# Kernel tuning notes

Hardware: AMD Instinct MI355X
Metric: run time of the kernel (lower is better)

## Reference

```python
import jax, jax.numpy as jnp
import numpy as np

HIDDEN = 768
TMPL = 128  # template tokens stripped from x/xi
LN_EPS = 1e-5


def _layernorm(h, gamma, beta):
    mu = jnp.mean(h, axis=-1, keepdims=True)
    var = jnp.mean((h - mu) ** 2, axis=-1, keepdims=True)
    return (h - mu) * jax.lax.rsqrt(var + LN_EPS) * gamma + beta


def setup_inputs() -> dict:
    key = jax.random.key(0)
    ks = jax.random.split(key, 7)
    B, NT, LX, C = 32, 320, 704, HIDDEN
    s = C ** -0.5  # scale params so activations stay O(1)
    return {
        "T": jax.random.normal(ks[0], (B, NT, C), jnp.float32),
        "x": jax.random.normal(ks[1], (B, LX, C), jnp.float32),
        "xi": jax.random.normal(ks[2], (B, LX, C), jnp.float32),
        "Wq": jax.random.normal(ks[3], (C, C), jnp.float32) * s,
        "Wk": jax.random.normal(ks[4], (C, C), jnp.float32) * s,
        "Wv": jax.random.normal(ks[5], (C, C), jnp.float32) * s,
        "Wout": jax.random.normal(ks[6], (C, C), jnp.float32) * s,
        "gamma": jnp.ones((C,), jnp.float32),
        "beta": jnp.zeros((C,), jnp.float32),
    }


def reference(T, x, xi, Wq, Wk, Wv, Wout, gamma, beta):
    scale = T.shape[-1] ** -0.5
    xs = x[:, TMPL:]    # [B, N, C]
    xis = xi[:, TMPL:]  # [B, N, C]

    q = jnp.einsum("btc,cd->btd", T, Wq)
    k = jnp.einsum("bnc,cd->bnd", xs, Wk)
    ki = jnp.einsum("bnc,cd->bnd", xis, Wk)
    v = jnp.einsum("bnc,cd->bnd", xs, Wv)
    vi = jnp.einsum("bnc,cd->bnd", xis, Wv)

    aw = jax.nn.softmax(jnp.einsum("btd,bnd->btn", q, k) * scale, axis=-1)   # [B,Nt,N]
    awi = jax.nn.softmax(jnp.einsum("btd,bnd->btn", q, ki) * scale, axis=-1)  # [B,Nt,N]

    D = aw - awi
    num_rows = jnp.float32(D.shape[1])
    ones_cnt = jnp.sum(D > 0, axis=1).astype(jnp.float32)   # [B,N]
    half_cnt = jnp.sum(D == 0, axis=1).astype(jnp.float32)  # [B,N]
    rgb_ratio = (ones_cnt / num_rows)[..., None]   # [B,N,1]
    eq_ratio = (half_cnt / num_rows)[..., None]    # [B,N,1]
    tir_ratio = 1.0 - rgb_ratio - eq_ratio

    x_s = v * (rgb_ratio + eq_ratio) + vi * (tir_ratio + eq_ratio)  # [B,N,C]

    x_out = jnp.einsum("btn,bnc->btc", aw, v) @ Wout
    xi_out = jnp.einsum("btn,bnc->btc", awi, vi) @ Wout
    T_new = _layernorm(T + x_out + xi_out, gamma, beta)
    return x_s, T_new
```

## Files before the change

kernel.cpp:

```cpp
#include <hip/hip_runtime.h>

#define BB   32
#define NT   320
#define LX   704
#define TMPL 128
#define NS   576
#define CC   768
#define NS2  1152
#define LN_EPS 1e-5f

typedef __attribute__((ext_vector_type(8))) short short8;
typedef __attribute__((ext_vector_type(4))) float f32x4;
typedef unsigned long long u64;

typedef __attribute__((address_space(3))) void as3_void;
typedef __attribute__((address_space(1))) void as1_void;
#define GLDS16(g, l) __builtin_amdgcn_global_load_lds((const as1_void*)(g), (as3_void*)(l), 16, 0, 0)

__device__ __forceinline__ unsigned short f2bf(float f) {
    union { float f; unsigned u; } v; v.f = f;
    unsigned r = v.u + 0x7FFFu + ((v.u >> 16) & 1u);
    return (unsigned short)(r >> 16);
}
__device__ __forceinline__ float bf2f(unsigned short h) {
    union { unsigned u; float f; } v; v.u = ((unsigned)h) << 16;
    return v.f;
}

__device__ __forceinline__ float block_sum256(float v) {
    __shared__ float sm[4];
    #pragma unroll
    for (int o = 32; o > 0; o >>= 1) v += __shfl_down(v, o, 64);
    __syncthreads();
    if ((threadIdx.x & 63) == 0) sm[threadIdx.x >> 6] = v;
    __syncthreads();
    return sm[0] + sm[1] + sm[2] + sm[3];
}
__device__ __forceinline__ float block_max256(float v) {
    __shared__ float sm[4];
    #pragma unroll
    for (int o = 32; o > 0; o >>= 1) v = fmaxf(v, __shfl_down(v, o, 64));
    __syncthreads();
    if ((threadIdx.x & 63) == 0) sm[threadIdx.x >> 6] = v;
    __syncthreads();
    return fmaxf(fmaxf(sm[0], sm[1]), fmaxf(sm[2], sm[3]));
}

template<bool F32OUT>
__device__ __forceinline__ void gemm64_core(const short* __restrict__ Ab,
                                            const short* __restrict__ Bb,
                                            void* __restrict__ Cb,
                                            int N, int K, float alpha)
{
    __shared__ short As[64 * 32];
    __shared__ short Bs[128 * 32];
    const int m0 = blockIdx.y * 64;
    const int n0 = blockIdx.x * 128;
    const int tid  = threadIdx.x;
    const int lane = tid & 63;
    const int w    = tid >> 6;
    const int wr   = (w >> 1) * 32;
    const int wc   = (w & 1) * 64;

    const int srow = tid >> 2;
    const int g    = ((tid & 3) ^ ((srow >> 1) & 3)) * 8;
    const short* gA  = Ab + (long)(m0 + srow) * K + g;
    const short* gB0 = Bb + (long)(n0 + srow) * K + g;
    const short* gB1 = gB0 + (long)64 * K;
    short* lA  = As + tid * 8;
    short* lB0 = Bs + tid * 8;
    short* lB1 = Bs + 2048 + tid * 8;

    const int fl = lane & 15;
    const int ch = lane >> 4;

    f32x4 acc[2][4] = {};

    for (int k0 = 0; k0 < K; k0 += 32) {
        GLDS16(gA  + k0, lA);
        GLDS16(gB0 + k0, lB0);
        GLDS16(gB1 + k0, lB1);
        __syncthreads();

        short8 af[2], bfv[4];
        #pragma unroll
        for (int mt = 0; mt < 2; ++mt) {
            int row = wr + mt * 16 + fl;
            af[mt] = *(const short8*)(As + row * 32 + ((ch ^ ((row >> 1) & 3)) * 8));
        }
        #pragma unroll
        for (int nt = 0; nt < 4; ++nt) {
            int row = wc + nt * 16 + fl;
            bfv[nt] = *(const short8*)(Bs + row * 32 + ((ch ^ ((row >> 1) & 3)) * 8));
        }
        #pragma unroll
        for (int mt = 0; mt < 2; ++mt)
            #pragma unroll
            for (int nt = 0; nt < 4; ++nt)
                acc[mt][nt] = __builtin_amdgcn_mfma_f32_16x16x32_bf16(
                    af[mt], bfv[nt], acc[mt][nt], 0, 0, 0);
        __syncthreads();
    }

    float* Cf = (float*)Cb;
    unsigned short* Ch = (unsigned short*)Cb;
    const int rq = (lane >> 4) * 4;
    #pragma unroll
    for (int mt = 0; mt < 2; ++mt) {
        #pragma unroll
        for (int r = 0; r < 4; ++r) {
            long ro = (long)(m0 + wr + mt * 16 + rq + r) * N + n0 + wc + fl;
            #pragma unroll
            for (int nt = 0; nt < 4; ++nt) {
                float val = acc[mt][nt][r] * alpha;
                if (F32OUT) Cf[ro + nt * 16] = val;
                else        Ch[ro + nt * 16] = f2bf(val);
            }
        }
    }
}

template<bool F32OUT>
__global__ __launch_bounds__(256) void gemm64(
    const short* __restrict__ A, const short* __restrict__ Bt, void* __restrict__ C,
    int N, int K, long sA, long sB, long sC, float alpha)
{
    const int b = blockIdx.z;
    void* Cb = F32OUT ? (void*)((float*)C + (long)b * sC)
                      : (void*)((unsigned short*)C + (long)b * sC);
    gemm64_core<F32OUT>(A + (long)b * sA, Bt + (long)b * sB, Cb, N, K, alpha);
}

__global__ __launch_bounds__(256) void proj4(
    const short* __restrict__ xsb, const short* __restrict__ xisb,
    const short* __restrict__ WkT, const short* __restrict__ WvT,
    unsigned short* __restrict__ kkb, unsigned short* __restrict__ vvb)
{
    const int which = blockIdx.z & 3;
    const int b     = blockIdx.z >> 2;
    const short* A  = ((which & 1) ? xisb : xsb) + (long)b * NS * CC;
    const short* Bt = (which & 2) ? WvT : WkT;
    unsigned short* C = ((which & 2) ? vvb : kkb)
                        + (long)b * NS2 * CC + (long)(which & 1) * NS * CC;
    gemm64_core<false>(A, Bt, C, CC, CC, 1.f);
}

__global__ void conv_in(const float* __restrict__ T, const float* __restrict__ x,
                        const float* __restrict__ xi,
                        unsigned short* __restrict__ Tb, unsigned short* __restrict__ xsb,
                        unsigned short* __restrict__ xisb)
{
    const int which = blockIdx.y;
    long i4 = ((long)blockIdx.x * 256 + threadIdx.x) * 4;
    const float* src; unsigned short* dst; long total; int rows, off, rpb;
    if (which == 0) { src = T;  dst = Tb;   total = (long)BB * NT * CC; rows = NT; off = 0;    rpb = NT; }
    else if (which == 1) { src = x;  dst = xsb;  total = (long)BB * NS * CC; rows = LX; off = TMPL; rpb = NS; }
    else            { src = xi; dst = xisb; total = (long)BB * NS * CC; rows = LX; off = TMPL; rpb = NS; }
    if (i4 >= total) return;
    int c   = (int)(i4 % CC);
    long rw = i4 / CC;
    int t   = (int)(rw % rpb);
    int b   = (int)(rw / rpb);
    const float4 f = *(const float4*)(src + ((long)b * rows + off + t) * CC + c);
    ushort4 o;
    o.x = f2bf(f.x); o.y = f2bf(f.y); o.z = f2bf(f.z); o.w = f2bf(f.w);
    *(ushort4*)(dst + i4) = o;
}

__global__ void conv_wt4(const float* __restrict__ Wq, const float* __restrict__ Wk,
                         const float* __restrict__ Wv, const float* __restrict__ Wo,
                         unsigned short* __restrict__ WqT, unsigned short* __restrict__ WkT,
                         unsigned short* __restrict__ WvT, unsigned short* __restrict__ WoT)
{
    const float* W; unsigned short* WT;
    switch (blockIdx.z) {
        case 0: W = Wq; WT = WqT; break;
        case 1: W = Wk; WT = WkT; break;
        case 2: W = Wv; WT = WvT; break;
        default: W = Wo; WT = WoT; break;
    }
    __shared__ float tile[32][33];
    const int c0 = blockIdx.x * 32, r0 = blockIdx.y * 32;
    const int tx = threadIdx.x & 31, ty = threadIdx.x >> 5;
    #pragma unroll
    for (int i = 0; i < 4; ++i)
        tile[ty + 8 * i][tx] = W[(long)(r0 + ty + 8 * i) * CC + c0 + tx];
    __syncthreads();
    #pragma unroll
    for (int i = 0; i < 4; ++i)
        WT[(long)(c0 + ty + 8 * i) * CC + r0 + tx] = f2bf(tile[tx][ty + 8 * i]);
}

__global__ void trans_vv(const unsigned short* __restrict__ vvb, unsigned short* __restrict__ vvT)
{
    __shared__ unsigned short tile[32][34];
    const int b = blockIdx.z;
    const int n0 = blockIdx.x * 32, c0 = blockIdx.y * 32;
    const int tx = threadIdx.x & 31, ty = threadIdx.x >> 5;
    const long ib = (long)b * NS2 * CC;
    #pragma unroll
    for (int i = 0; i < 4; ++i)
        tile[ty + 8 * i][tx] = vvb[ib + (long)(n0 + ty + 8 * i) * CC + c0 + tx];
    __syncthreads();
    #pragma unroll
    for (int i = 0; i < 4; ++i)
        vvT[ib + (long)(c0 + ty + 8 * i) * NS2 + n0 + tx] = tile[tx][ty + 8 * i];
}

__global__ void softmax_pack(const float* __restrict__ P, unsigned short* __restrict__ Pb,
                             u64* __restrict__ posm, u64* __restrict__ eqm)
{
    const long r = blockIdx.x;
    const float* p = P + r * NS2;
    const int tid = threadIdx.x;

    float a0 = p[tid], a1 = p[tid + 256], a2 = (tid < 64) ? p[tid + 512] : -1e30f;
    float m1 = block_max256(fmaxf(fmaxf(a0, a1), a2));
    float e0 = __expf(a0 - m1), e1 = __expf(a1 - m1), e2 = (tid < 64) ? __expf(a2 - m1) : 0.f;
    float s1 = block_sum256(e0 + e1 + e2);
    float i1 = 1.f / s1;
    e0 *= i1; e1 *= i1; e2 *= i1;

    const float* q = p + NS;
    float b0 = q[tid], b1 = q[tid + 256], b2 = (tid < 64) ? q[tid + 512] : -1e30f;
    float m2 = block_max256(fmaxf(fmaxf(b0, b1), b2));
    float f0 = __expf(b0 - m2), f1 = __expf(b1 - m2), f2v = (tid < 64) ? __expf(b2 - m2) : 0.f;
    float s2 = block_sum256(f0 + f1 + f2v);
    float i2 = 1.f / s2;
    f0 *= i2; f1 *= i2; f2v *= i2;

    unsigned short* ob = Pb + r * NS2;
    ob[tid] = f2bf(e0); ob[tid + 256] = f2bf(e1);
    if (tid < 64) ob[tid + 512] = f2bf(e2);
    ob[NS + tid] = f2bf(f0); ob[NS + tid + 256] = f2bf(f1);
    if (tid < 64) ob[NS + tid + 512] = f2bf(f2v);

    u64* pm = posm + r * 9;
    u64* em = eqm  + r * 9;
    const int wv = tid >> 6;
    float d0 = e0 - f0, d1 = e1 - f1, d2 = e2 - f2v;
    u64 P0 = __ballot(d0 > 0.f), E0 = __ballot(d0 == 0.f);
    if ((tid & 63) == 0) { pm[wv] = P0; em[wv] = E0; }
    u64 P1 = __ballot(d1 > 0.f), E1 = __ballot(d1 == 0.f);
    if ((tid & 63) == 0) { pm[4 + wv] = P1; em[4 + wv] = E1; }
    u64 P2 = __ballot(tid < 64 && d2 > 0.f), E2 = __ballot(tid < 64 && d2 == 0.f);
    if (tid == 0) { pm[8] = P2; em[8] = E2; }
}

__global__ void xs_fused(const u64* __restrict__ posm, const u64* __restrict__ eqm,
                         const unsigned short* __restrict__ vvb, float* __restrict__ out)
{
    const int gid = blockIdx.x;
    const int b = gid / NS, n = gid - b * NS;
    const int tid = threadIdx.x;
    const int wsel = n >> 6, bit = n & 63;
    float ones = 0.f, eqc = 0.f;
    for (int t = tid; t < NT; t += 256) {
        long o = ((long)(b * NT + t)) * 9 + wsel;
        ones += (float)((posm[o] >> bit) & 1);
        eqc  += (float)((eqm[o]  >> bit) & 1);
    }
    ones = block_sum256(ones);
    eqc  = block_sum256(eqc);
    float rgb = ones * (1.f / NT), e = eqc * (1.f / NT);
    float c1 = rgb + e;
    float c2 = (1.f - rgb - e) + e;
    const unsigned* pv  = (const unsigned*)(vvb + ((long)b * NS2 + n) * CC);
    const unsigned* pvi = (const unsigned*)(vvb + ((long)b * NS2 + n + NS) * CC);
    float* po = out + ((long)b * NS + n) * CC;
    for (int idx = tid; idx < CC / 2; idx += 256) {
        unsigned a = pv[idx], bb = pvi[idx];
        float2 o2;
        o2.x = bf2f((unsigned short)(a & 0xFFFF)) * c1 + bf2f((unsigned short)(bb & 0xFFFF)) * c2;
        o2.y = bf2f((unsigned short)(a >> 16))    * c1 + bf2f((unsigned short)(bb >> 16))    * c2;
        *(float2*)(po + 2 * idx) = o2;
    }
}

__global__ void add_ln(const float* __restrict__ T, const float* __restrict__ S2,
                       const float* __restrict__ gamma, const float* __restrict__ beta,
                       float* __restrict__ out)
{
    const long r = blockIdx.x;
    const int tid = threadIdx.x;
    const float* tp = T  + r * CC;
    const float* sp = S2 + r * CC;
    float h[3];
    float sum = 0.f;
    #pragma unroll
    for (int i = 0; i < 3; ++i) {
        h[i] = tp[tid + 256 * i] + sp[tid + 256 * i];
        sum += h[i];
    }
    sum = block_sum256(sum);
    float mu = sum * (1.f / CC);
    float varp = 0.f;
    #pragma unroll
    for (int i = 0; i < 3; ++i) { float d = h[i] - mu; varp += d * d; }
    varp = block_sum256(varp);
    float inv = rsqrtf(varp * (1.f / CC) + LN_EPS);
    #pragma unroll
    for (int i = 0; i < 3; ++i) {
        int c = tid + 256 * i;
        out[r * CC + c] = (h[i] - mu) * inv * gamma[c] + beta[c];
    }
}

extern "C" void kernel_launch(void* const* d_in, const int* in_sizes, int n_in,
                              void* d_out, int out_size, void* d_ws, size_t ws_size,
                              hipStream_t stream) {
    const float* T     = (const float*)d_in[0];
    const float* x     = (const float*)d_in[1];
    const float* xi    = (const float*)d_in[2];
    const float* Wq    = (const float*)d_in[3];
    const float* Wk    = (const float*)d_in[4];
    const float* Wv    = (const float*)d_in[5];
    const float* Wout  = (const float*)d_in[6];
    const float* gamma = (const float*)d_in[7];
    const float* beta  = (const float*)d_in[8];
    float* out = (float*)d_out;

    const long B_T  = (long)BB * NT * CC * 2;
    const long B_KK = (long)BB * NS2 * CC * 2;
    const long B_WT = (long)CC * CC * 2;
    const long B_XS = (long)BB * NS * CC * 2;
    const long B_PB = (long)BB * NT * NS2 * 2;
    const long B_MK = (long)BB * NT * 9 * 8;

    char* cur = (char*)d_ws;
    unsigned short* Tb   = (unsigned short*)cur; cur += B_T;
    unsigned short* qb   = (unsigned short*)cur; cur += B_T;
    unsigned short* kkb  = (unsigned short*)cur; cur += B_KK;
    unsigned short* WqT  = (unsigned short*)cur; cur += B_WT;
    unsigned short* WkT  = (unsigned short*)cur; cur += B_WT;
    unsigned short* WvT  = (unsigned short*)cur; cur += B_WT;
    unsigned short* WoT  = (unsigned short*)cur; cur += B_WT;
    unsigned short* vvb  = (unsigned short*)cur; cur += B_KK;
    unsigned short* vvT  = (unsigned short*)cur; cur += B_KK;
    unsigned short* xsb  = (unsigned short*)cur;
    unsigned short* xisb = xsb + (long)BB * NS * CC;  cur += 2 * B_XS;
    unsigned short* Pb   = (unsigned short*)cur; cur += B_PB;
    u64* posm            = (u64*)cur; cur += B_MK;
    u64* eqm             = (u64*)cur; cur += B_MK;
    if ((size_t)(cur - (char*)d_ws) > ws_size) return;

    float* P  = (float*)xsb;
    unsigned short* Sb = Tb;
    float* S2 = (float*)vvb;

    const float scale = 1.0f / sqrtf((float)CC);
    dim3 blk(256);

    conv_in<<<dim3((BB * NS * CC) / 1024, 3), blk, 0, stream>>>(T, x, xi, Tb, xsb, xisb);
    conv_wt4<<<dim3(CC / 32, CC / 32, 4), blk, 0, stream>>>(Wq, Wk, Wv, Wout, WqT, WkT, WvT, WoT);

    proj4<<<dim3(CC / 128, NS / 64, BB * 4), blk, 0, stream>>>(
        (const short*)xsb, (const short*)xisb, (const short*)WkT, (const short*)WvT, kkb, vvb);

    gemm64<false><<<dim3(CC / 128, NT / 64, BB), blk, 0, stream>>>(
        (const short*)Tb, (const short*)WqT, qb, CC, CC,
        (long)NT * CC, 0, (long)NT * CC, 1.f);

    trans_vv<<<dim3(NS2 / 32, CC / 32, BB), blk, 0, stream>>>(vvb, vvT);

    gemm64<true><<<dim3(NS2 / 128, NT / 64, BB), blk, 0, stream>>>(
        (const short*)qb, (const short*)kkb, P, NS2, CC,
        (long)NT * CC, (long)NS2 * CC, (long)NT * NS2, scale);

    softmax_pack<<<BB * NT, blk, 0, stream>>>(P, Pb, posm, eqm);

    xs_fused<<<BB * NS, blk, 0, stream>>>(posm, eqm, vvb, out);

    gemm64<false><<<dim3(CC / 128, NT / 64, BB), blk, 0, stream>>>(
        (const short*)Pb, (const short*)vvT, Sb, CC, NS2,
        (long)NT * NS2, (long)CC * NS2, (long)NT * CC, 1.f);

    gemm64<true><<<dim3(CC / 128, NT / 64, BB), blk, 0, stream>>>(
        (const short*)Sb, (const short*)WoT, S2, CC, CC,
        (long)NT * CC, 0, (long)NT * CC, 1.f);

    add_ln<<<BB * NT, blk, 0, stream>>>(T, S2, gamma, beta, out + (long)BB * NS * CC);
}
```

Baseline: 663.9 us.

## Use 128x128 tiled GEMMs with batch folded into M for weight projections

Adds a 128x128-tile bf16 MFMA GEMM core with swizzled LDS staging through direct global-to-LDS loads. The Q projection and the output projection now treat all batches as one tall matrix instead of batched 64-row tiles. K and V for both x and xi are fused into a single GEMM over the stacked rows and concatenated Wk/Wv weights, with the rows scattered back into the per-batch layout. The aim is more data reuse per tile and fewer, larger launches; the fusion relies on WkT and WvT sitting next to each other in the workspace.

```diff
diff --git a/kernel.cpp b/kernel.cpp
--- a/kernel.cpp
+++ b/kernel.cpp
@@ -131,18 +131,123 @@
     gemm64_core<F32OUT>(A + (long)b * sA, Bt + (long)b * sB, Cb, N, K, alpha);
 }
 
-__global__ __launch_bounds__(256) void proj4(
-    const short* __restrict__ xsb, const short* __restrict__ xisb,
-    const short* __restrict__ WkT, const short* __restrict__ WvT,
+__device__ __forceinline__ void gemm128_acc(const short* __restrict__ Ab,
+                                            const short* __restrict__ Bb,
+                                            int K, f32x4 acc[4][4])
+{
+    __shared__ short As[128 * 32];
+    __shared__ short Bs[128 * 32];
+    const int tid  = threadIdx.x;
+    const int lane = tid & 63;
+    const int w    = tid >> 6;
+    const int wr   = (w >> 1) * 64;
+    const int wc   = (w & 1) * 64;
+
+    const int srow = tid >> 2;
+    const int g    = ((tid & 3) ^ ((srow >> 1) & 3)) * 8;
+    const short* gA0 = Ab + (long)srow * K + g;
+    const short* gA1 = gA0 + (long)64 * K;
+    const short* gB0 = Bb + (long)srow * K + g;
+    const short* gB1 = gB0 + (long)64 * K;
+    short* lA0 = As + tid * 8;
+    short* lA1 = As + 2048 + tid * 8;
+    short* lB0 = Bs + tid * 8;
+    short* lB1 = Bs + 2048 + tid * 8;
+
+    const int fl = lane & 15;
+    const int ch = lane >> 4;
+
+    for (int k0 = 0; k0 < K; k0 += 32) {
+        GLDS16(gA0 + k0, lA0);
+        GLDS16(gA1 + k0, lA1);
+        GLDS16(gB0 + k0, lB0);
+        GLDS16(gB1 + k0, lB1);
+        __syncthreads();
+
+        short8 af[4], bfv[4];
+        #pragma unroll
+        for (int mt = 0; mt < 4; ++mt) {
+            int row = wr + mt * 16 + fl;
+            af[mt] = *(const short8*)(As + row * 32 + ((ch ^ ((row >> 1) & 3)) * 8));
+        }
+        #pragma unroll
+        for (int nt = 0; nt < 4; ++nt) {
+            int row = wc + nt * 16 + fl;
+            bfv[nt] = *(const short8*)(Bs + row * 32 + ((ch ^ ((row >> 1) & 3)) * 8));
+        }
+        #pragma unroll
+        for (int mt = 0; mt < 4; ++mt)
+            #pragma unroll
+            for (int nt = 0; nt < 4; ++nt)
+                acc[mt][nt] = __builtin_amdgcn_mfma_f32_16x16x32_bf16(
+                    af[mt], bfv[nt], acc[mt][nt], 0, 0, 0);
+        __syncthreads();
+    }
+}
+
+template<bool F32OUT>
+__global__ __launch_bounds__(256) void gemm128(
+    const short* __restrict__ A, const short* __restrict__ Bt, void* __restrict__ C,
+    int N, int K, float alpha)
+{
+    const int n0 = blockIdx.x * 128;
+    const int m0 = blockIdx.y * 128;
+    f32x4 acc[4][4] = {};
+    gemm128_acc(A + (long)m0 * K, Bt + (long)n0 * K, K, acc);
+
+    const int tid = threadIdx.x, lane = tid & 63, w = tid >> 6;
+    const int wr = (w >> 1) * 64, wc = (w & 1) * 64;
+    const int fl = lane & 15, rq = (lane >> 4) * 4;
+    float* Cf = (float*)C;
+    unsigned short* Ch = (unsigned short*)C;
+    #pragma unroll
+    for (int mt = 0; mt < 4; ++mt) {
+        #pragma unroll
+        for (int r = 0; r < 4; ++r) {
+            long ro = (long)(m0 + wr + mt * 16 + rq + r) * N + n0 + wc + fl;
+            #pragma unroll
+            for (int nt = 0; nt < 4; ++nt) {
+                float val = acc[mt][nt][r] * alpha;
+                if (F32OUT) Cf[ro + nt * 16] = val;
+                else        Ch[ro + nt * 16] = f2bf(val);
+            }
+        }
+    }
+}
+
+__global__ __launch_bounds__(256) void proj_kv(
+    const short* __restrict__ X, const short* __restrict__ WkvT,
     unsigned short* __restrict__ kkb, unsigned short* __restrict__ vvb)
 {
-    const int which = blockIdx.z & 3;
-    const int b     = blockIdx.z >> 2;
-    const short* A  = ((which & 1) ? xisb : xsb) + (long)b * NS * CC;
-    const short* Bt = (which & 2) ? WvT : WkT;
-    unsigned short* C = ((which & 2) ? vvb : kkb)
-                        + (long)b * NS2 * CC + (long)(which & 1) * NS * CC;
-    gemm64_core<false>(A, Bt, C, CC, CC, 1.f);
+    const int n0 = blockIdx.x * 128;
+    const int m0 = blockIdx.y * 128;
+    f32x4 acc[4][4] = {};
+    gemm128_acc(X + (long)m0 * CC, WkvT + (long)n0 * CC, CC, acc);
+
+    const int tid = threadIdx.x, lane = tid & 63, w = tid >> 6;
+    const int wr = (w >> 1) * 64, wc = (w & 1) * 64;
+    const int fl = lane & 15, rq = (lane >> 4) * 4;
+
+    unsigned short* base = (n0 < CC) ? kkb : vvb;
+    const int j0 = ((n0 < CC) ? n0 : n0 - CC) + wc + fl;
+
+    #pragma unroll
+    for (int mt = 0; mt < 4; ++mt) {
+        #pragma unroll
+        for (int r = 0; r < 4; ++r) {
+            int row = m0 + wr + mt * 16 + rq + r;
+            int isxi = (row >= BB * NS) ? 1 : 0;
+            int r2 = row - isxi * (BB * NS);
+            int b = r2 / NS;
+            int n = r2 - b * NS;
+            unsigned short* po = base + (long)b * NS2 * CC
+                                      + (long)isxi * NS * CC
+                                      + (long)n * CC + j0;
+            #pragma unroll
+            for (int nt = 0; nt < 4; ++nt)
+                po[nt * 16] = f2bf(acc[mt][nt][r]);
+        }
+    }
 }
 
 __global__ void conv_in(const float* __restrict__ T, const float* __restrict__ x,
@@ -354,12 +459,11 @@
     conv_in<<<dim3((BB * NS * CC) / 1024, 3), blk, 0, stream>>>(T, x, xi, Tb, xsb, xisb);
     conv_wt4<<<dim3(CC / 32, CC / 32, 4), blk, 0, stream>>>(Wq, Wk, Wv, Wout, WqT, WkT, WvT, WoT);
 
-    proj4<<<dim3(CC / 128, NS / 64, BB * 4), blk, 0, stream>>>(
-        (const short*)xsb, (const short*)xisb, (const short*)WkT, (const short*)WvT, kkb, vvb);
-
-    gemm64<false><<<dim3(CC / 128, NT / 64, BB), blk, 0, stream>>>(
-        (const short*)Tb, (const short*)WqT, qb, CC, CC,
-        (long)NT * CC, 0, (long)NT * CC, 1.f);
+    proj_kv<<<dim3((2 * CC) / 128, (2 * BB * NS) / 128), blk, 0, stream>>>(
+        (const short*)xsb, (const short*)WkT, kkb, vvb);
+
+    gemm128<false><<<dim3(CC / 128, (BB * NT) / 128), blk, 0, stream>>>(
+        (const short*)Tb, (const short*)WqT, qb, CC, CC, 1.f);
 
     trans_vv<<<dim3(NS2 / 32, CC / 32, BB), blk, 0, stream>>>(vvb, vvT);
 
@@ -375,9 +479,8 @@
         (const short*)Pb, (const short*)vvT, Sb, CC, NS2,
         (long)NT * NS2, (long)CC * NS2, (long)NT * CC, 1.f);
 
-    gemm64<true><<<dim3(CC / 128, NT / 64, BB), blk, 0, stream>>>(
-        (const short*)Sb, (const short*)WoT, S2, CC, CC,
-        (long)NT * CC, 0, (long)NT * CC, 1.f);
+    gemm128<true><<<dim3(CC / 128, (BB * NT) / 128), blk, 0, stream>>>(
+        (const short*)Sb, (const short*)WoT, S2, CC, CC, 1.f);
 
     add_ln<<<BB * NT, blk, 0, stream>>>(T, S2, gamma, beta, out + (long)BB * NS * CC);
 }
```

Result: faster. 630.1 us (-5.1%).
